# Performance work log

Measured on AMD Instinct MI355X. Metric: run time of the kernel, lower is better.

The kernel has to match this reference:

```python
import jax, jax.numpy as jnp
import numpy as np

B, T, C = 1, 4096, 1024   # batch, seq, n_embd
E, K = 64, 8              # num_experts, router top-k
G, TG = 8, 4              # n_group, topk_group
H, HS = 512, 2048         # expert hidden, shared-expert hidden
STD = 0.02


def setup_inputs() -> dict:
    key = jax.random.key(0)
    ks = jax.random.split(key, 9)
    return {
        "x": jax.random.normal(ks[0], (B, T, C), jnp.float32),
        "router_w": jax.random.normal(ks[1], (E, C), jnp.float32) * (C ** -0.5),
        "e_bias": jnp.zeros((E,), jnp.float32),  # e_score_correction_bias buffer
        "gate_w": jax.random.normal(ks[2], (E, C, H), jnp.float32) * STD,
        "up_w": jax.random.normal(ks[3], (E, C, H), jnp.float32) * STD,
        "down_w": jax.random.normal(ks[4], (E, H, C), jnp.float32) * STD,
        "sh_gate_w": jax.random.normal(ks[5], (C, HS), jnp.float32) * STD,
        "sh_up_w": jax.random.normal(ks[6], (C, HS), jnp.float32) * STD,
        "sh_down_w": jax.random.normal(ks[7], (HS, C), jnp.float32) * STD,
    }


def _route(xf, router_w, e_bias):
    # grouped sigmoid top-k routing with score-correction bias (group_limited_greedy)
    S = xf.shape[0]
    scores = jax.nn.sigmoid(xf @ router_w.T)          # [S,E], raw sigmoid scores
    sb = scores + e_bias                               # biased scores (selection only)
    epg = E // G
    # per-group score = sum of top (K // topk_group) biased scores in that group
    grp = jax.lax.top_k(sb.reshape(S, G, epg), K // TG)[0].sum(-1)   # [S,G]
    gidx = jax.lax.top_k(grp, TG)[1]                                 # [S,TG]
    gmask = jnp.zeros((S, G), bool).at[jnp.arange(S)[:, None], gidx].set(True)
    emask = jnp.repeat(gmask, epg, axis=1)                           # [S,E]
    masked = jnp.where(emask, sb, -jnp.inf)
    topk_idx = jax.lax.top_k(masked, K)[1]                           # [S,K]
    w = jnp.take_along_axis(scores, topk_idx, axis=1)                # raw scores gathered
    w = w / (w.sum(-1, keepdims=True) + 1e-20)                       # norm_topk_prob
    return topk_idx, w


def reference(x, router_w, e_bias, gate_w, up_w, down_w, sh_gate_w, sh_up_w, sh_down_w):
    Bq, Tq, Cq = x.shape
    xf = x.reshape(Bq * Tq, Cq)
    # always-on shared expert (SwiGLU)
    shared = (jax.nn.silu(xf @ sh_gate_w) * (xf @ sh_up_w)) @ sh_down_w
    topk_idx, w = _route(xf, router_w, e_bias)
    fe = topk_idx.reshape(-1)                          # [S*K] expert id per routed row
    order = jnp.argsort(fe, stable=True)               # sort rows by expert (grouped)
    tok = order // K                                   # source token of each sorted row
    sorted_x = xf[tok]                                 # [S*K, C]
    group_sizes = jnp.bincount(fe, length=E).astype(jnp.int32)
    # grouped GEMMs (== torch._grouped_mm / bmm-over-buckets in the original)
    g = jax.lax.ragged_dot(sorted_x, gate_w, group_sizes)
    u = jax.lax.ragged_dot(sorted_x, up_w, group_sizes)
    h = jax.nn.silu(g) * u
    o = jax.lax.ragged_dot(h, down_w, group_sizes)     # [S*K, C]
    o = o * w.reshape(-1)[order][:, None]              # weight by routing prob
    routed = jnp.zeros_like(xf).at[tok].add(o)         # combine back per token
    return (shared + routed).reshape(Bq, Tq, Cq)
```

## Files before the change

### kernel.cpp

```cpp
#include <hip/hip_runtime.h>
#include <hip/hip_bf16.h>
#include <stdint.h>


#define S_TOK 4096
#define C_DIM 1024
#define E_NUM 64
#define H_DIM 512
#define HS_DIM 2048
#define ROWS_TOTAL (S_TOK * 8)

typedef __attribute__((ext_vector_type(8))) short short8;
typedef __attribute__((ext_vector_type(4))) float f32x4;

static __device__ __forceinline__ unsigned short f2bf(float f) {
    union { float f; uint32_t u; } v; v.f = f;
    uint32_t u = v.u;
    u += 0x7fffu + ((u >> 16) & 1u);
    return (unsigned short)(u >> 16);
}

static __device__ __forceinline__ void gl2lds16(const void* g, void* l) {
    __builtin_amdgcn_global_load_lds(
        (const __attribute__((address_space(1))) uint32_t*)g,
        (__attribute__((address_space(3))) uint32_t*)l, 16, 0, 0);
}

__global__ __launch_bounds__(256)
void router_scores_k(const float* __restrict__ x, const float* __restrict__ rw,
                     float* __restrict__ scores) {
    int t0 = blockIdx.x * 32;
    __shared__ float xs[32][36];
    __shared__ float wsm[64][36];
    int t = threadIdx.x;
    int tx = t & 15, ty = t >> 4;
    float acc[2][4] = {};
    for (int k0 = 0; k0 < C_DIM; k0 += 32) {
        {
            int r = t >> 3, c = t & 7;
            *(float4*)&xs[r][c * 4] = *(const float4*)(x + (size_t)(t0 + r) * C_DIM + k0 + c * 4);
        }
        #pragma unroll
        for (int i = 0; i < 2; i++) {
            int idx = t + 256 * i;
            int r = idx >> 3, c = idx & 7;
            *(float4*)&wsm[r][c * 4] = *(const float4*)(rw + (size_t)r * C_DIM + k0 + c * 4);
        }
        __syncthreads();
        #pragma unroll
        for (int kk = 0; kk < 32; kk += 4) {
            float4 a0 = *(const float4*)&xs[ty * 2 + 0][kk];
            float4 a1 = *(const float4*)&xs[ty * 2 + 1][kk];
            #pragma unroll
            for (int j = 0; j < 4; j++) {
                float4 b = *(const float4*)&wsm[tx * 4 + j][kk];
                acc[0][j] += a0.x * b.x + a0.y * b.y + a0.z * b.z + a0.w * b.w;
                acc[1][j] += a1.x * b.x + a1.y * b.y + a1.z * b.z + a1.w * b.w;
            }
        }
        __syncthreads();
    }
    #pragma unroll
    for (int i = 0; i < 2; i++)
        #pragma unroll
        for (int j = 0; j < 4; j++)
            scores[(size_t)(t0 + ty * 2 + i) * E_NUM + tx * 4 + j] =
                1.f / (1.f + __expf(-acc[i][j]));
}

__global__ __launch_bounds__(256)
void topk_k(const float* __restrict__ scores, const float* __restrict__ ebias,
            int* __restrict__ topk_idx, float* __restrict__ topk_w,
            int* __restrict__ counts) {
    int t = blockIdx.x * 4 + (threadIdx.x >> 6);
    int e = threadIdx.x & 63;
    float sc = scores[(size_t)t * E_NUM + e];
    float sb = sc + ebias[e];
    float m1 = sb, m2 = -1e30f;
    #pragma unroll
    for (int off = 1; off <= 4; off <<= 1) {
        float o1 = __shfl_xor(m1, off);
        float o2 = __shfl_xor(m2, off);
        float hi = fmaxf(m1, o1), lo = fminf(m1, o1);
        m2 = fmaxf(lo, fmaxf(m2, o2));
        m1 = hi;
    }
    float grp = m1 + m2;
    float grpv[8];
    #pragma unroll
    for (int g = 0; g < 8; g++) grpv[g] = __shfl(grp, g * 8);
    unsigned gsel = 0;
    #pragma unroll
    for (int k = 0; k < 4; k++) {
        float best = -1e30f; int bi = 0;
        #pragma unroll
        for (int g = 0; g < 8; g++)
            if (!((gsel >> g) & 1) && grpv[g] > best) { best = grpv[g]; bi = g; }
        gsel |= 1u << bi;
    }
    float val = ((gsel >> (e >> 3)) & 1) ? sb : -1e30f;
    int idx[8]; float sv[8]; float wsum = 0.f;
    #pragma unroll
    for (int k = 0; k < 8; k++) {
        uint32_t u = __float_as_uint(val);
        uint32_t mu = (u & 0x80000000u) ? ~u : (u | 0x80000000u);
        unsigned long long key = ((unsigned long long)mu << 6) | (unsigned long long)(63 - e);
        #pragma unroll
        for (int off = 32; off; off >>= 1) {
            unsigned long long ok = __shfl_xor(key, off);
            if (ok > key) key = ok;
        }
        int win = 63 - (int)(key & 63ull);
        idx[k] = win;
        sv[k] = __shfl(sc, win);
        wsum += sv[k];
        if (e == win) val = -1e30f;
    }
    float inv = 1.f / (wsum + 1e-20f);
    if (e < 8) {
        topk_idx[t * 8 + e] = idx[e];
        topk_w[t * 8 + e] = sv[e] * inv;
        atomicAdd(&counts[idx[e]], 1);
    }
}

__global__ void zero_counts_k(int* counts) { counts[threadIdx.x] = 0; }

__global__ void scan_k(const int* __restrict__ counts, int* __restrict__ base,
                       int* __restrict__ cursor) {
    int e = threadIdx.x;
    int c = counts[e];
    int s = c;
    #pragma unroll
    for (int off = 1; off < 64; off <<= 1) {
        int o = __shfl_up(s, off);
        if (e >= off) s += o;
    }
    int ex = s - c;
    base[e] = ex;
    cursor[e] = ex;
}

__global__ void scatter_k(const int* __restrict__ topk_idx, const float* __restrict__ topk_w,
                          int* __restrict__ cursor, int* __restrict__ row_token,
                          float* __restrict__ row_wgt, int* __restrict__ pos_of) {
    int i = blockIdx.x * blockDim.x + threadIdx.x;
    int e = topk_idx[i];
    int pos = atomicAdd(&cursor[e], 1);
    row_token[pos] = i >> 3;
    row_wgt[pos] = topk_w[i];
    pos_of[i] = pos;
}

__global__ __launch_bounds__(256)
void combine_k(const float* __restrict__ O, const int* __restrict__ pos_of,
               float* __restrict__ out) {
    int t = blockIdx.x;
    int c = threadIdx.x;
    float4 s = ((const float4*)(out + (size_t)t * C_DIM))[c];
    int p[8];
    #pragma unroll
    for (int k = 0; k < 8; k++) p[k] = pos_of[t * 8 + k];
    #pragma unroll
    for (int k = 0; k < 8; k++) {
        float4 v = ((const float4*)(O + (size_t)p[k] * C_DIM))[c];
        s.x += v.x; s.y += v.y; s.z += v.z; s.w += v.w;
    }
    ((float4*)(out + (size_t)t * C_DIM))[c] = s;
}

__global__ void cvt_bf16_k(const float* __restrict__ in, unsigned short* __restrict__ out, int n8) {
    int i = blockIdx.x * blockDim.x + threadIdx.x;
    if (i >= n8) return;
    float4 v0 = ((const float4*)in)[2 * i];
    float4 v1 = ((const float4*)in)[2 * i + 1];
    unsigned short t[8] = { f2bf(v0.x), f2bf(v0.y), f2bf(v0.z), f2bf(v0.w),
                            f2bf(v1.x), f2bf(v1.y), f2bf(v1.z), f2bf(v1.w) };
    ((uint4*)out)[i] = *(uint4*)t;
}

#define TP 69
__global__ __launch_bounds__(256)
void transpose_k(const float* __restrict__ in, unsigned short* __restrict__ out, int R, int C) {
    size_t bofs = (size_t)blockIdx.z * R * C;
    in += bofs; out += bofs;
    int r0 = blockIdx.y * 64, c0 = blockIdx.x * 64;
    __shared__ float T[64 * TP];
    int t = threadIdx.x;
    int cg = t & 15, rg = t >> 4;
    #pragma unroll
    for (int ii = 0; ii < 4; ii++) {
        float4 v = *(const float4*)(in + (size_t)(r0 + rg * 4 + ii) * C + c0 + cg * 4);
        T[(cg * 4 + 0) * TP + rg * 4 + ii] = v.x;
        T[(cg * 4 + 1) * TP + rg * 4 + ii] = v.y;
        T[(cg * 4 + 2) * TP + rg * 4 + ii] = v.z;
        T[(cg * 4 + 3) * TP + rg * 4 + ii] = v.w;
    }
    __syncthreads();
    int n = t >> 2, ks = (t & 3) * 16;
    unsigned short h[16];
    #pragma unroll
    for (int u = 0; u < 16; u++) h[u] = f2bf(T[n * TP + ks + u]);
    unsigned short* op = out + (size_t)(c0 + n) * R + r0 + ks;
    *(uint4*)op = *(uint4*)&h[0];
    *(uint4*)(op + 8) = *(uint4*)&h[8];
}

template<bool FUSED, bool GATHER, bool GROUPED, int EPI>
__global__ __launch_bounds__(256, 2)
void gemm2_k(const short* __restrict__ A, const short* __restrict__ B1t,
             const short* __restrict__ B2t, void* __restrict__ Cout,
             int M, int N, int K,
             const int* __restrict__ counts, const int* __restrict__ base,
             const int* __restrict__ row_token, const float* __restrict__ row_wgt) {
    int e = GROUPED ? blockIdx.z : 0;
    int Mrows = GROUPED ? counts[e] : M;
    int n0 = blockIdx.x * 128;
    int rowbase = GROUPED ? base[e] : 0;
    const short* B1 = B1t + (GROUPED ? (size_t)e * N * K : 0) + (size_t)n0 * K;
    const short* B2 = FUSED ? (B2t + (GROUPED ? (size_t)e * N * K : 0) + (size_t)n0 * K) : nullptr;

    __shared__ short As[3 * 4096];
    __shared__ short Bs1[3 * 4096];
    __shared__ short Bs2[FUSED ? 3 * 4096 : 16];

    int tid = threadIdx.x;
    int lane = tid & 63, w = tid >> 6;
    int wr = w >> 1, wc = w & 1;
    int quad = lane >> 4, l16 = lane & 15;
    int sr = lane >> 2, sc = lane & 3;

    for (int m0 = blockIdx.y * 128; m0 < Mrows; m0 += gridDim.y * 128) {
        const short* aptr[2];
        const short* b1ptr[2];
        const short* b2ptr[2];
        #pragma unroll
        for (int i = 0; i < 2; i++) {
            int row = w * 32 + i * 16 + sr;
            int mrow = m0 + row;
            int cl = mrow < Mrows ? mrow : (Mrows - 1);
            size_t arow;
            if (GATHER)       arow = (size_t)row_token[rowbase + cl];
            else if (GROUPED) arow = (size_t)(rowbase + cl);
            else              arow = (size_t)mrow;
            aptr[i] = A + arow * K + sc * 8;
            b1ptr[i] = B1 + (size_t)row * K + sc * 8;
            if (FUSED) b2ptr[i] = B2 + (size_t)row * K + sc * 8;
        }

        f32x4 acc1[4][4] = {};
        f32x4 acc2[4][4] = {};

        const int nk = K >> 5;
        auto stage = [&](int slot) {
            #pragma unroll
            for (int i = 0; i < 2; i++) {
                int lb = slot * 4096 + (w * 32 + i * 16) * 32;
                gl2lds16(aptr[i], &As[lb]);   aptr[i] += 32;
                gl2lds16(b1ptr[i], &Bs1[lb]); b1ptr[i] += 32;
                if (FUSED) { gl2lds16(b2ptr[i], &Bs2[lb]); b2ptr[i] += 32; }
            }
        };
        stage(0);
        if (nk > 1) stage(1);

        int slot = 0, nslot = 2;
        for (int t = 0; t < nk; t++) {
            if (t + 1 < nk) {
                if constexpr (FUSED) asm volatile("s_waitcnt vmcnt(6)" ::: "memory");
                else                 asm volatile("s_waitcnt vmcnt(4)" ::: "memory");
            } else {
                asm volatile("s_waitcnt vmcnt(0)" ::: "memory");
            }
            __builtin_amdgcn_s_barrier();
            __builtin_amdgcn_sched_barrier(0);

            if (t + 2 < nk) stage(nslot);

            int bofs = slot * 4096;
            short8 a[4], b1[4], b2[4];
            #pragma unroll
            for (int i = 0; i < 4; i++)
                a[i] = *(const short8*)&As[bofs + (wr * 64 + i * 16 + l16) * 32 + quad * 8];
            #pragma unroll
            for (int j = 0; j < 4; j++) {
                b1[j] = *(const short8*)&Bs1[bofs + (wc * 64 + j * 16 + l16) * 32 + quad * 8];
                if (FUSED)
                    b2[j] = *(const short8*)&Bs2[bofs + (wc * 64 + j * 16 + l16) * 32 + quad * 8];
            }
            #pragma unroll
            for (int i = 0; i < 4; i++)
                #pragma unroll
                for (int j = 0; j < 4; j++) {
                    acc1[i][j] = __builtin_amdgcn_mfma_f32_16x16x32_bf16(a[i], b1[j], acc1[i][j], 0, 0, 0);
                    if (FUSED)
                        acc2[i][j] = __builtin_amdgcn_mfma_f32_16x16x32_bf16(a[i], b2[j], acc2[i][j], 0, 0, 0);
                }
            slot = (slot == 2) ? 0 : slot + 1;
            nslot = (nslot == 2) ? 0 : nslot + 1;
        }

        #pragma unroll
        for (int i = 0; i < 4; i++) {
            #pragma unroll
            for (int rr = 0; rr < 4; rr++) {
                int row = m0 + wr * 64 + i * 16 + quad * 4 + rr;
                if (row >= Mrows) continue;
                size_t orow = GROUPED ? (size_t)(rowbase + row) : (size_t)row;
                float scl = 0.f;
                if (EPI == 2) scl = row_wgt[rowbase + row];
                #pragma unroll
                for (int j = 0; j < 4; j++) {
                    int n = n0 + wc * 64 + j * 16 + l16;
                    float v = acc1[i][j][rr];
                    if (EPI == 0) {
                        float u = acc2[i][j][rr];
                        float h = v / (1.f + __expf(-v)) * u;
                        ((unsigned short*)Cout)[orow * N + n] = f2bf(h);
                    } else if (EPI == 1) {
                        ((float*)Cout)[orow * N + n] = v;
                    } else {
                        ((float*)Cout)[orow * N + n] = v * scl;
                    }
                }
            }
        }
        __syncthreads();
    }
}

extern "C" void kernel_launch(void* const* d_in, const int* in_sizes, int n_in,
                              void* d_out, int out_size, void* d_ws, size_t ws_size,
                              hipStream_t stream) {
    const float* x        = (const float*)d_in[0];
    const float* router_w = (const float*)d_in[1];
    const float* e_bias   = (const float*)d_in[2];
    const float* gate_w   = (const float*)d_in[3];
    const float* up_w     = (const float*)d_in[4];
    const float* down_w   = (const float*)d_in[5];
    const float* sh_gate  = (const float*)d_in[6];
    const float* sh_up    = (const float*)d_in[7];
    const float* sh_down  = (const float*)d_in[8];
    float* out = (float*)d_out;
    char* ws = (char*)d_ws;

    int*   counts    = (int*)(ws);
    int*   base      = (int*)(ws + 256);
    int*   cursor    = (int*)(ws + 512);
    int*   topk_idx  = (int*)(ws + 1024);
    float* topk_w    = (float*)(ws + 1024 + 131072);
    int*   row_token = (int*)(ws + 1024 + 2 * 131072);
    float* row_wgt   = (float*)(ws + 1024 + 3 * 131072);
    float* scoresbuf = (float*)(ws + 1024 + 4 * 131072);
    int*   pos_of    = (int*)(ws + 1664 * 1024);
    const size_t MB = 1u << 20;
    unsigned short* xb        = (unsigned short*)(ws + 2 * MB);
    unsigned short* Hs        = (unsigned short*)(ws + 10 * MB);
    unsigned short* Hr        = (unsigned short*)(ws + 26 * MB);
    unsigned short* sh_gate_t = (unsigned short*)(ws + 58 * MB);
    unsigned short* sh_up_t   = (unsigned short*)(ws + 62 * MB);
    unsigned short* sh_down_t = (unsigned short*)(ws + 66 * MB);
    unsigned short* gate_t    = (unsigned short*)(ws + 70 * MB);
    unsigned short* up_t      = (unsigned short*)(ws + 134 * MB);
    unsigned short* down_t    = (unsigned short*)(ws + 198 * MB);
    float* O = (float*)(ws + 70 * MB);

    zero_counts_k<<<1, 64, 0, stream>>>(counts);
    router_scores_k<<<S_TOK / 32, 256, 0, stream>>>(x, router_w, scoresbuf);
    topk_k<<<S_TOK / 4, 256, 0, stream>>>(scoresbuf, e_bias, topk_idx, topk_w, counts);
    scan_k<<<1, 64, 0, stream>>>(counts, base, cursor);
    scatter_k<<<ROWS_TOTAL / 256, 256, 0, stream>>>(topk_idx, topk_w, cursor, row_token, row_wgt, pos_of);

    cvt_bf16_k<<<S_TOK * C_DIM / 8 / 256, 256, 0, stream>>>(x, xb, S_TOK * C_DIM / 8);
    transpose_k<<<dim3(HS_DIM / 64, C_DIM / 64, 1), 256, 0, stream>>>(sh_gate, sh_gate_t, C_DIM, HS_DIM);
    transpose_k<<<dim3(HS_DIM / 64, C_DIM / 64, 1), 256, 0, stream>>>(sh_up,   sh_up_t,   C_DIM, HS_DIM);
    transpose_k<<<dim3(C_DIM / 64, HS_DIM / 64, 1), 256, 0, stream>>>(sh_down, sh_down_t, HS_DIM, C_DIM);
    transpose_k<<<dim3(H_DIM / 64, C_DIM / 64, E_NUM), 256, 0, stream>>>(gate_w, gate_t, C_DIM, H_DIM);
    transpose_k<<<dim3(H_DIM / 64, C_DIM / 64, E_NUM), 256, 0, stream>>>(up_w,   up_t,   C_DIM, H_DIM);
    transpose_k<<<dim3(C_DIM / 64, H_DIM / 64, E_NUM), 256, 0, stream>>>(down_w, down_t, H_DIM, C_DIM);

    gemm2_k<true, false, false, 0><<<dim3(HS_DIM / 128, S_TOK / 128, 1), 256, 0, stream>>>(
        (const short*)xb, (const short*)sh_gate_t, (const short*)sh_up_t, Hs,
        S_TOK, HS_DIM, C_DIM, nullptr, nullptr, nullptr, nullptr);
    gemm2_k<false, false, false, 1><<<dim3(C_DIM / 128, S_TOK / 128, 1), 256, 0, stream>>>(
        (const short*)Hs, (const short*)sh_down_t, nullptr, out,
        S_TOK, C_DIM, HS_DIM, nullptr, nullptr, nullptr, nullptr);

    gemm2_k<true, true, true, 0><<<dim3(H_DIM / 128, 4, E_NUM), 256, 0, stream>>>(
        (const short*)xb, (const short*)gate_t, (const short*)up_t, Hr,
        0, H_DIM, C_DIM, counts, base, row_token, row_wgt);
    gemm2_k<false, false, true, 2><<<dim3(C_DIM / 128, 4, E_NUM), 256, 0, stream>>>(
        (const short*)Hr, (const short*)down_t, nullptr, O,
        0, C_DIM, H_DIM, counts, base, row_token, row_wgt);

    combine_k<<<S_TOK, 256, 0, stream>>>(O, pos_of, out);
}
```

Baseline: 994.6 us.

## Schedule grouped expert GEMMs from a flat tile work list built in scan

The scan kernel now also emits a flat list of (expert, m-tile) pairs, with a prefix sum over per-expert tile counts and unused slots marked -1. The routed GEMMs launch one block column per list entry, replacing the fixed four y-blocks per expert that looped over that expert's m-tiles. The aim is to balance load when experts get uneven token counts and to remove the serial tile loop and its trailing barrier. In exchange it launches up to 320 tile rows, some of which exit at once, and needs an extra indirection load at block start.

New measurement: 950.1 us. -4.5%, faster.

```diff
diff --git a/kernel.cpp b/kernel.cpp
--- a/kernel.cpp
+++ b/kernel.cpp
@@ -9,6 +9,7 @@
 #define H_DIM 512
 #define HS_DIM 2048
 #define ROWS_TOTAL (S_TOK * 8)
+#define T_TILES 320
 
 typedef __attribute__((ext_vector_type(8))) short short8;
 typedef __attribute__((ext_vector_type(4))) float f32x4;
@@ -127,7 +128,8 @@
 __global__ void zero_counts_k(int* counts) { counts[threadIdx.x] = 0; }
 
 __global__ void scan_k(const int* __restrict__ counts, int* __restrict__ base,
-                       int* __restrict__ cursor) {
+                       int* __restrict__ cursor, int* __restrict__ tile_e,
+                       int* __restrict__ tile_m0) {
     int e = threadIdx.x;
     int c = counts[e];
     int s = c;
@@ -139,6 +141,17 @@
     int ex = s - c;
     base[e] = ex;
     cursor[e] = ex;
+    int nt = (c + 127) >> 7;
+    int ts = nt;
+    #pragma unroll
+    for (int off = 1; off < 64; off <<= 1) {
+        int o = __shfl_up(ts, off);
+        if (e >= off) ts += o;
+    }
+    int tb = ts - nt;
+    for (int i = 0; i < nt; i++) { tile_e[tb + i] = e; tile_m0[tb + i] = i * 128; }
+    int total = __shfl(ts, 63);
+    for (int j = total + e; j < T_TILES; j += 64) tile_e[j] = -1;
 }
 
 __global__ void scatter_k(const int* __restrict__ topk_idx, const float* __restrict__ topk_w,
@@ -206,19 +219,28 @@
     *(uint4*)(op + 8) = *(uint4*)&h[8];
 }
 
-template<bool FUSED, bool GATHER, bool GROUPED, int EPI>
+template<bool FUSED, bool GATHER, bool WL, int EPI>
 __global__ __launch_bounds__(256, 2)
 void gemm2_k(const short* __restrict__ A, const short* __restrict__ B1t,
              const short* __restrict__ B2t, void* __restrict__ Cout,
              int M, int N, int K,
              const int* __restrict__ counts, const int* __restrict__ base,
-             const int* __restrict__ row_token, const float* __restrict__ row_wgt) {
-    int e = GROUPED ? blockIdx.z : 0;
-    int Mrows = GROUPED ? counts[e] : M;
+             const int* __restrict__ row_token, const float* __restrict__ row_wgt,
+             const int* __restrict__ tile_e, const int* __restrict__ tile_m0) {
+    int e = 0, m0, Mrows, rowbase = 0;
+    if (WL) {
+        e = tile_e[blockIdx.y];
+        if (e < 0) return;
+        m0 = tile_m0[blockIdx.y];
+        Mrows = counts[e];
+        rowbase = base[e];
+    } else {
+        m0 = blockIdx.y * 128;
+        Mrows = M;
+    }
     int n0 = blockIdx.x * 128;
-    int rowbase = GROUPED ? base[e] : 0;
-    const short* B1 = B1t + (GROUPED ? (size_t)e * N * K : 0) + (size_t)n0 * K;
-    const short* B2 = FUSED ? (B2t + (GROUPED ? (size_t)e * N * K : 0) + (size_t)n0 * K) : nullptr;
+    const short* B1 = B1t + (WL ? (size_t)e * N * K : 0) + (size_t)n0 * K;
+    const short* B2 = FUSED ? (B2t + (WL ? (size_t)e * N * K : 0) + (size_t)n0 * K) : nullptr;
 
     __shared__ short As[3 * 4096];
     __shared__ short Bs1[3 * 4096];
@@ -230,102 +252,99 @@
     int quad = lane >> 4, l16 = lane & 15;
     int sr = lane >> 2, sc = lane & 3;
 
-    for (int m0 = blockIdx.y * 128; m0 < Mrows; m0 += gridDim.y * 128) {
-        const short* aptr[2];
-        const short* b1ptr[2];
-        const short* b2ptr[2];
+    const short* aptr[2];
+    const short* b1ptr[2];
+    const short* b2ptr[2];
+    #pragma unroll
+    for (int i = 0; i < 2; i++) {
+        int row = w * 32 + i * 16 + sr;
+        int mrow = m0 + row;
+        int cl = mrow < Mrows ? mrow : (Mrows - 1);
+        size_t arow;
+        if (GATHER)  arow = (size_t)row_token[rowbase + cl];
+        else if (WL) arow = (size_t)(rowbase + cl);
+        else         arow = (size_t)mrow;
+        aptr[i] = A + arow * K + sc * 8;
+        b1ptr[i] = B1 + (size_t)row * K + sc * 8;
+        if (FUSED) b2ptr[i] = B2 + (size_t)row * K + sc * 8;
+    }
+
+    f32x4 acc1[4][4] = {};
+    f32x4 acc2[4][4] = {};
+
+    const int nk = K >> 5;
+    auto stage = [&](int slot) {
         #pragma unroll
         for (int i = 0; i < 2; i++) {
-            int row = w * 32 + i * 16 + sr;
-            int mrow = m0 + row;
-            int cl = mrow < Mrows ? mrow : (Mrows - 1);
-            size_t arow;
-            if (GATHER)       arow = (size_t)row_token[rowbase + cl];
-            else if (GROUPED) arow = (size_t)(rowbase + cl);
-            else              arow = (size_t)mrow;
-            aptr[i] = A + arow * K + sc * 8;
-            b1ptr[i] = B1 + (size_t)row * K + sc * 8;
-            if (FUSED) b2ptr[i] = B2 + (size_t)row * K + sc * 8;
-        }
-
-        f32x4 acc1[4][4] = {};
-        f32x4 acc2[4][4] = {};
-
-        const int nk = K >> 5;
-        auto stage = [&](int slot) {
-            #pragma unroll
-            for (int i = 0; i < 2; i++) {
-                int lb = slot * 4096 + (w * 32 + i * 16) * 32;
-                gl2lds16(aptr[i], &As[lb]);   aptr[i] += 32;
-                gl2lds16(b1ptr[i], &Bs1[lb]); b1ptr[i] += 32;
-                if (FUSED) { gl2lds16(b2ptr[i], &Bs2[lb]); b2ptr[i] += 32; }
-            }
-        };
-        stage(0);
-        if (nk > 1) stage(1);
-
-        int slot = 0, nslot = 2;
-        for (int t = 0; t < nk; t++) {
-            if (t + 1 < nk) {
-                if constexpr (FUSED) asm volatile("s_waitcnt vmcnt(6)" ::: "memory");
-                else                 asm volatile("s_waitcnt vmcnt(4)" ::: "memory");
-            } else {
-                asm volatile("s_waitcnt vmcnt(0)" ::: "memory");
-            }
-            __builtin_amdgcn_s_barrier();
-            __builtin_amdgcn_sched_barrier(0);
-
-            if (t + 2 < nk) stage(nslot);
-
-            int bofs = slot * 4096;
-            short8 a[4], b1[4], b2[4];
-            #pragma unroll
-            for (int i = 0; i < 4; i++)
-                a[i] = *(const short8*)&As[bofs + (wr * 64 + i * 16 + l16) * 32 + quad * 8];
+            int lb = slot * 4096 + (w * 32 + i * 16) * 32;
+            gl2lds16(aptr[i], &As[lb]);   aptr[i] += 32;
+            gl2lds16(b1ptr[i], &Bs1[lb]); b1ptr[i] += 32;
+            if (FUSED) { gl2lds16(b2ptr[i], &Bs2[lb]); b2ptr[i] += 32; }
+        }
+    };
+    stage(0);
+    if (nk > 1) stage(1);
+
+    int slot = 0, nslot = 2;
+    for (int t = 0; t < nk; t++) {
+        if (t + 1 < nk) {
+            if constexpr (FUSED) asm volatile("s_waitcnt vmcnt(6)" ::: "memory");
+            else                 asm volatile("s_waitcnt vmcnt(4)" ::: "memory");
+        } else {
+            asm volatile("s_waitcnt vmcnt(0)" ::: "memory");
+        }
+        __builtin_amdgcn_s_barrier();
+        __builtin_amdgcn_sched_barrier(0);
+
+        if (t + 2 < nk) stage(nslot);
+
+        int bofs = slot * 4096;
+        short8 a[4], b1[4], b2[4];
+        #pragma unroll
+        for (int i = 0; i < 4; i++)
+            a[i] = *(const short8*)&As[bofs + (wr * 64 + i * 16 + l16) * 32 + quad * 8];
+        #pragma unroll
+        for (int j = 0; j < 4; j++) {
+            b1[j] = *(const short8*)&Bs1[bofs + (wc * 64 + j * 16 + l16) * 32 + quad * 8];
+            if (FUSED)
+                b2[j] = *(const short8*)&Bs2[bofs + (wc * 64 + j * 16 + l16) * 32 + quad * 8];
+        }
+        #pragma unroll
+        for (int i = 0; i < 4; i++)
             #pragma unroll
             for (int j = 0; j < 4; j++) {
-                b1[j] = *(const short8*)&Bs1[bofs + (wc * 64 + j * 16 + l16) * 32 + quad * 8];
+                acc1[i][j] = __builtin_amdgcn_mfma_f32_16x16x32_bf16(a[i], b1[j], acc1[i][j], 0, 0, 0);
                 if (FUSED)
-                    b2[j] = *(const short8*)&Bs2[bofs + (wc * 64 + j * 16 + l16) * 32 + quad * 8];
+                    acc2[i][j] = __builtin_amdgcn_mfma_f32_16x16x32_bf16(a[i], b2[j], acc2[i][j], 0, 0, 0);
             }
+        slot = (slot == 2) ? 0 : slot + 1;
+        nslot = (nslot == 2) ? 0 : nslot + 1;
+    }
+
+    #pragma unroll
+    for (int i = 0; i < 4; i++) {
+        #pragma unroll
+        for (int rr = 0; rr < 4; rr++) {
+            int row = m0 + wr * 64 + i * 16 + quad * 4 + rr;
+            if (row >= Mrows) continue;
+            size_t orow = WL ? (size_t)(rowbase + row) : (size_t)row;
+            float scl = 0.f;
+            if (EPI == 2) scl = row_wgt[rowbase + row];
             #pragma unroll
-            for (int i = 0; i < 4; i++)
-                #pragma unroll
-                for (int j = 0; j < 4; j++) {
-                    acc1[i][j] = __builtin_amdgcn_mfma_f32_16x16x32_bf16(a[i], b1[j], acc1[i][j], 0, 0, 0);
-                    if (FUSED)
-                        acc2[i][j] = __builtin_amdgcn_mfma_f32_16x16x32_bf16(a[i], b2[j], acc2[i][j], 0, 0, 0);
-                }
-            slot = (slot == 2) ? 0 : slot + 1;
-            nslot = (nslot == 2) ? 0 : nslot + 1;
-        }
-
-        #pragma unroll
-        for (int i = 0; i < 4; i++) {
-            #pragma unroll
-            for (int rr = 0; rr < 4; rr++) {
-                int row = m0 + wr * 64 + i * 16 + quad * 4 + rr;
-                if (row >= Mrows) continue;
-                size_t orow = GROUPED ? (size_t)(rowbase + row) : (size_t)row;
-                float scl = 0.f;
-                if (EPI == 2) scl = row_wgt[rowbase + row];
-                #pragma unroll
-                for (int j = 0; j < 4; j++) {
-                    int n = n0 + wc * 64 + j * 16 + l16;
-                    float v = acc1[i][j][rr];
-                    if (EPI == 0) {
-                        float u = acc2[i][j][rr];
-                        float h = v / (1.f + __expf(-v)) * u;
-                        ((unsigned short*)Cout)[orow * N + n] = f2bf(h);
-                    } else if (EPI == 1) {
-                        ((float*)Cout)[orow * N + n] = v;
-                    } else {
-                        ((float*)Cout)[orow * N + n] = v * scl;
-                    }
+            for (int j = 0; j < 4; j++) {
+                int n = n0 + wc * 64 + j * 16 + l16;
+                float v = acc1[i][j][rr];
+                if (EPI == 0) {
+                    float u = acc2[i][j][rr];
+                    float h = v / (1.f + __expf(-v)) * u;
+                    ((unsigned short*)Cout)[orow * N + n] = f2bf(h);
+                } else if (EPI == 1) {
+                    ((float*)Cout)[orow * N + n] = v;
+                } else {
+                    ((float*)Cout)[orow * N + n] = v * scl;
                 }
             }
         }
-        __syncthreads();
     }
 }
 
@@ -353,6 +372,8 @@
     float* row_wgt   = (float*)(ws + 1024 + 3 * 131072);
     float* scoresbuf = (float*)(ws + 1024 + 4 * 131072);
     int*   pos_of    = (int*)(ws + 1664 * 1024);
+    int*   tile_e    = (int*)(ws + 1800 * 1024);
+    int*   tile_m0   = (int*)(ws + 1808 * 1024);
     const size_t MB = 1u << 20;
     unsigned short* xb        = (unsigned short*)(ws + 2 * MB);
     unsigned short* Hs        = (unsigned short*)(ws + 10 * MB);
@@ -368,7 +389,7 @@
     zero_counts_k<<<1, 64, 0, stream>>>(counts);
     router_scores_k<<<S_TOK / 32, 256, 0, stream>>>(x, router_w, scoresbuf);
     topk_k<<<S_TOK / 4, 256, 0, stream>>>(scoresbuf, e_bias, topk_idx, topk_w, counts);
-    scan_k<<<1, 64, 0, stream>>>(counts, base, cursor);
+    scan_k<<<1, 64, 0, stream>>>(counts, base, cursor, tile_e, tile_m0);
     scatter_k<<<ROWS_TOTAL / 256, 256, 0, stream>>>(topk_idx, topk_w, cursor, row_token, row_wgt, pos_of);
 
     cvt_bf16_k<<<S_TOK * C_DIM / 8 / 256, 256, 0, stream>>>(x, xb, S_TOK * C_DIM / 8);
@@ -381,17 +402,17 @@
 
     gemm2_k<true, false, false, 0><<<dim3(HS_DIM / 128, S_TOK / 128, 1), 256, 0, stream>>>(
         (const short*)xb, (const short*)sh_gate_t, (const short*)sh_up_t, Hs,
-        S_TOK, HS_DIM, C_DIM, nullptr, nullptr, nullptr, nullptr);
+        S_TOK, HS_DIM, C_DIM, nullptr, nullptr, nullptr, nullptr, nullptr, nullptr);
     gemm2_k<false, false, false, 1><<<dim3(C_DIM / 128, S_TOK / 128, 1), 256, 0, stream>>>(
         (const short*)Hs, (const short*)sh_down_t, nullptr, out,
-        S_TOK, C_DIM, HS_DIM, nullptr, nullptr, nullptr, nullptr);
-
-    gemm2_k<true, true, true, 0><<<dim3(H_DIM / 128, 4, E_NUM), 256, 0, stream>>>(
+        S_TOK, C_DIM, HS_DIM, nullptr, nullptr, nullptr, nullptr, nullptr, nullptr);
+
+    gemm2_k<true, true, true, 0><<<dim3(H_DIM / 128, T_TILES, 1), 256, 0, stream>>>(
         (const short*)xb, (const short*)gate_t, (const short*)up_t, Hr,
-        0, H_DIM, C_DIM, counts, base, row_token, row_wgt);
-    gemm2_k<false, false, true, 2><<<dim3(C_DIM / 128, 4, E_NUM), 256, 0, stream>>>(
+        0, H_DIM, C_DIM, counts, base, row_token, row_wgt, tile_e, tile_m0);
+    gemm2_k<false, false, true, 2><<<dim3(C_DIM / 128, T_TILES, 1), 256, 0, stream>>>(
         (const short*)Hr, (const short*)down_t, nullptr, O,
-        0, C_DIM, H_DIM, counts, base, row_token, row_wgt);
+        0, C_DIM, H_DIM, counts, base, row_token, row_wgt, tile_e, tile_m0);
 
     combine_k<<<S_TOK, 256, 0, stream>>>(O, pos_of, out);
 }
```
